# Kernel tuning notes

Measured on AMD Instinct MI355X. Metric: run time of the kernel, lower is better.

The kernel has to match this reference:

```python
import jax, jax.numpy as jnp
import numpy as np

CLAMP = 1e-4


def setup_inputs() -> dict:
    key = jax.random.key(0)
    k1, k2 = jax.random.split(key)
    B, C, H, W = 8, 21, 512, 512
    pred = jax.random.normal(k1, (B, C, H, W), dtype=jnp.float32)
    # valid labels are 1..C-1 (0 = background skipped; class C never appears,
    # matching the original code's loop-with-skip behavior)
    label = jax.random.randint(k2, (B, H, W), 1, C, dtype=jnp.int32)
    return {"pred": pred, "label": label}


def _lovasz(pred, label):
    num_classes = pred.shape[1]
    # [B,C,H,W] -> [N, C], sigmoid + clamp
    p = jnp.transpose(pred, (0, 2, 3, 1)).reshape(-1, num_classes)
    p = jnp.clip(jax.nn.sigmoid(p.astype(jnp.float32)), CLAMP, 1.0 - CLAMP)
    lab = label.reshape(-1)

    # classes 1..num_classes-1 (class num_classes is never present in labels,
    # so its iteration in the original loop always hits `continue`)
    classes = jnp.arange(1, num_classes)
    masks = (lab[None, :] == classes[:, None]).astype(jnp.float32)  # [C-1, N]
    preds_c = p[:, 1:num_classes].T                                  # [C-1, N]

    errors = jnp.abs(masks - preds_c)                                # [C-1, N]
    order = jnp.argsort(-errors, axis=1)                             # descending
    errors_sorted = jnp.take_along_axis(errors, order, axis=1)
    masks_sorted = jnp.take_along_axis(masks, order, axis=1)

    # lovasz_grad, vectorized over classes
    gts = jnp.sum(masks_sorted, axis=1, keepdims=True)               # [C-1, 1]
    intersection = gts - jnp.cumsum(masks_sorted, axis=1)
    union = gts + jnp.cumsum(1.0 - masks_sorted, axis=1)
    jac = 1.0 - intersection / union
    jac = jnp.concatenate([jac[:, :1], jac[:, 1:] - jac[:, :-1]], axis=1)

    per_class = jnp.sum(errors_sorted * jac, axis=1)                 # [C-1]
    present = gts[:, 0] > 0
    count = jnp.sum(present.astype(jnp.float32))
    return jnp.sum(jnp.where(present, per_class, 0.0)) / count


def reference(pred, label):
    return _lovasz(pred, label)
```

## Files before the change

### kernel.cpp

```cpp
#include <hip/hip_runtime.h>

#define NBINS  128
#define NCLS   20
#define CDIM   21
#define HW     (512 * 512)
#define NPIX   (8 * HW)
#define NCHUNK 512
#define CHUNK  (NPIX / NCHUNK)
#define HSZ    (NCLS * NBINS)
#define XSCALE 10.6666667f
#define XBIAS  64.0f

__device__ __forceinline__ float4 gld_f4(const float* p) {
    float4 r;
    asm volatile("global_load_dwordx4 %0, %1, off" : "=v"(r) : "v"(p));
    return r;
}
__device__ __forceinline__ int4 gld_i4(const int* p) {
    int4 r;
    asm volatile("global_load_dwordx4 %0, %1, off" : "=v"(r) : "v"(p));
    return r;
}

__global__ __launch_bounds__(512, 4) void lovasz_hist(const float* __restrict__ pred,
                                                      const int* __restrict__ label,
                                                      unsigned* __restrict__ g_part) {
    __shared__ unsigned s_hist[HSZ];
    const int tid = threadIdx.x;

    const long base = (long)blockIdx.x * CHUNK;
    const int  b    = (int)(base / HW);
    const long hw0  = base - (long)b * HW;
    const float* pbase = pred + ((long)b * CDIM + 1) * HW + hw0 + tid * 4;
    const int*   q     = label + base + tid * 4;

    int4 l[2];
    l[0] = gld_i4(q);
    l[1] = gld_i4(q + 2048);
    float4 buf[3][5];
#pragma unroll
    for (int gg = 0; gg < 2; ++gg)
#pragma unroll
        for (int k = 0; k < 5; ++k)
            buf[gg][k] = gld_f4(pbase + (long)(gg * 5 + k) * HW);

    for (int i = tid; i < HSZ; i += 512) s_hist[i] = 0u;
    __syncthreads();

    auto compute5 = [&](const float4* x, int cbase, const int4& lab) {
#pragma unroll
        for (int j = 0; j < 4; ++j) {
            const int lv = (j == 0) ? lab.x : (j == 1) ? lab.y : (j == 2) ? lab.z : lab.w;
#pragma unroll
            for (int k = 0; k < 5; ++k) {
                const float xv = (j == 0) ? x[k].x : (j == 1) ? x[k].y
                               : (j == 2) ? x[k].z : x[k].w;
                const bool  pos = (lv == cbase + k + 1);
                const float t   = pos ? -xv : xv;
                const float bf  = fminf(fmaxf(__builtin_fmaf(t, XSCALE, XBIAS), 0.0f), 127.0f);
                const int   bin = (int)bf;
                atomicAdd(&s_hist[(cbase + k) * NBINS + bin], pos ? 0x10001u : 1u);
            }
        }
    };

#pragma unroll
    for (int g = 0; g < 8; ++g) {
        if (g + 2 < 8) {
            const int gg = g + 2;
#pragma unroll
            for (int k = 0; k < 5; ++k)
                buf[gg % 3][k] =
                    gld_f4(pbase + (long)((gg & 3) * 5 + k) * HW + (gg >> 2) * 2048);
        }
        if (g < 6)       asm volatile("s_waitcnt vmcnt(10)" ::: "memory");
        else if (g == 6) asm volatile("s_waitcnt vmcnt(5)" ::: "memory");
        else             asm volatile("s_waitcnt vmcnt(0)" ::: "memory");
        __builtin_amdgcn_sched_barrier(0);
        compute5(buf[g % 3], (g & 3) * 5, l[g >> 2]);
    }

    __syncthreads();

    unsigned* gp = g_part + (size_t)blockIdx.x * HSZ;
    for (int i = tid; i < HSZ; i += 512) gp[i] = s_hist[i];
}

__global__ __launch_bounds__(256) void lovasz_reduce(const unsigned* __restrict__ g_part,
                                                     unsigned long long* __restrict__ H) {
    const int t  = threadIdx.x;
    const int i  = blockIdx.x * 16 + (t & 15);
    const int rc = t >> 4;
    const unsigned* gp = g_part + i;

    unsigned vc = 0, vp = 0;
#pragma unroll
    for (int bt = 0; bt < 4; ++bt) {
        unsigned pk = 0;
#pragma unroll
        for (int k = 0; k < 8; ++k)
            pk += gp[(size_t)(rc * 32 + bt * 8 + k) * HSZ];
        vc += pk & 0xFFFFu;
        vp += pk >> 16;
    }
    __shared__ unsigned s_c[16][16], s_p[16][16];
    s_c[rc][t & 15] = vc;
    s_p[rc][t & 15] = vp;
    __syncthreads();
    if (t < 16) {
        unsigned c = 0, p = 0;
#pragma unroll
        for (int r = 0; r < 16; ++r) { c += s_c[r][t]; p += s_p[r][t]; }
        H[blockIdx.x * 16 + t] = (unsigned long long)c | ((unsigned long long)p << 32);
    }
}

__global__ __launch_bounds__(1024) void lovasz_scan(const unsigned long long* __restrict__ H,
                                                    float* __restrict__ out) {
    __shared__ float cls_sum[NCLS];
    __shared__ float cls_cnt[NCLS];
    const int wid  = threadIdx.x >> 6;
    const int lane = threadIdx.x & 63;

#pragma unroll
    for (int it = 0; it < 2; ++it) {
        const int cls = it * 16 + wid;
        if (cls < NCLS) {
            const int bin_lo = 126 - 2 * lane;
            const ulonglong2 v = *reinterpret_cast<const ulonglong2*>(H + cls * NBINS + bin_lo);
            const int vc1 = (int)(v.x & 0xFFFFFFFFull), vp1 = (int)(v.x >> 32);
            const int vc0 = (int)(v.y & 0xFFFFFFFFull), vp0 = (int)(v.y >> 32);
            const int sc = vc0 + vc1, sp = vp0 + vp1;
            int ic = sc, ip = sp;
#pragma unroll
            for (int d = 1; d < 64; d <<= 1) {
                const int tc = __shfl_up(ic, d, 64);
                const int tp = __shfl_up(ip, d, 64);
                if (lane >= d) { ic += tc; ip += tp; }
            }
            const int G   = __shfl(ip, 63, 64);
            const int ec0 = ic - sc, ep0 = ip - sp;
            float contrib = 0.0f;
            if (G > 0) {
                const float fG = (float)G;
                auto J = [&](int i, int m) {
                    return 1.0f - (fG - (float)m) / (fG + (float)(i - m));
                };
                auto EMID = [&](int bn) {
                    const float xm = ((float)bn + 0.5f) * (12.0f / (float)NBINS) - 6.0f;
                    return 1.0f / (1.0f + __expf(-xm));
                };
                if (vc0) {
                    contrib += EMID(127 - 2 * lane) *
                               (J(ec0 + vc0, ep0 + vp0) - J(ec0, ep0));
                }
                if (vc1) {
                    const int ec = ec0 + vc0, ep = ep0 + vp0;
                    contrib += EMID(126 - 2 * lane) *
                               (J(ec + vc1, ep + vp1) - J(ec, ep));
                }
            }
#pragma unroll
            for (int d = 32; d > 0; d >>= 1) contrib += __shfl_down(contrib, d, 64);
            if (lane == 0) {
                cls_sum[cls] = contrib;
                cls_cnt[cls] = (G > 0) ? 1.0f : 0.0f;
            }
        }
    }
    __syncthreads();
    if (threadIdx.x == 0) {
        float s = 0.0f, n = 0.0f;
        for (int c = 0; c < NCLS; ++c) { s += cls_sum[c]; n += cls_cnt[c]; }
        out[0] = s / n;
    }
}

extern "C" void kernel_launch(void* const* d_in, const int* in_sizes, int n_in,
                              void* d_out, int out_size, void* d_ws, size_t ws_size,
                              hipStream_t stream) {
    const float* pred  = (const float*)d_in[0];
    const int*   label = (const int*)d_in[1];

    unsigned* g_part = (unsigned*)d_ws;
    unsigned long long* H = (unsigned long long*)(g_part + (size_t)NCHUNK * HSZ);
    float* out = (float*)d_out;

    lovasz_hist<<<NCHUNK, 512, 0, stream>>>(pred, label, g_part);
    lovasz_reduce<<<HSZ / 16, 256, 0, stream>>>(g_part, H);
    lovasz_scan<<<1, 1024, 0, stream>>>(H, out);
}
```

Measured before the change: 39.99 us.

## Double chunk count, fuse scan into reduce via last-block ticket

The histogram kernel now uses 1024 chunks of one pixel group each, with a two-buffer prefetch and a higher occupancy hint. The reduce kernel uses 320 blocks of 8 bins each, and the last block to finish, chosen by an atomic ticket counter, runs the per-class scan and final average. This drops one kernel launch. The counter is reset by block 0 of the histogram kernel. Trade-offs are twice as many partial histograms to read and write in the reduce, plus fence and atomic overhead.

After: 82.97 us. +107.5%, slower.

```diff
diff --git a/kernel.cpp b/kernel.cpp
--- a/kernel.cpp
+++ b/kernel.cpp
@@ -5,9 +5,10 @@
 #define CDIM   21
 #define HW     (512 * 512)
 #define NPIX   (8 * HW)
-#define NCHUNK 512
+#define NCHUNK 1024
 #define CHUNK  (NPIX / NCHUNK)
 #define HSZ    (NCLS * NBINS)
+#define NRED   320
 #define XSCALE 10.6666667f
 #define XBIAS  64.0f
 
@@ -22,22 +23,21 @@
     return r;
 }
 
-__global__ __launch_bounds__(512, 4) void lovasz_hist(const float* __restrict__ pred,
+__global__ __launch_bounds__(512, 6) void lovasz_hist(const float* __restrict__ pred,
                                                       const int* __restrict__ label,
-                                                      unsigned* __restrict__ g_part) {
+                                                      unsigned* __restrict__ g_part,
+                                                      unsigned* __restrict__ ctr) {
     __shared__ unsigned s_hist[HSZ];
     const int tid = threadIdx.x;
+    if (blockIdx.x == 0 && tid == 0) ctr[0] = 0u;
 
     const long base = (long)blockIdx.x * CHUNK;
     const int  b    = (int)(base / HW);
     const long hw0  = base - (long)b * HW;
     const float* pbase = pred + ((long)b * CDIM + 1) * HW + hw0 + tid * 4;
-    const int*   q     = label + base + tid * 4;
 
-    int4 l[2];
-    l[0] = gld_i4(q);
-    l[1] = gld_i4(q + 2048);
-    float4 buf[3][5];
+    const int4 l = gld_i4(label + base + tid * 4);
+    float4 buf[2][5];
 #pragma unroll
     for (int gg = 0; gg < 2; ++gg)
 #pragma unroll
@@ -47,10 +47,10 @@
     for (int i = tid; i < HSZ; i += 512) s_hist[i] = 0u;
     __syncthreads();
 
-    auto compute5 = [&](const float4* x, int cbase, const int4& lab) {
+    auto compute5 = [&](const float4* x, int cbase) {
 #pragma unroll
         for (int j = 0; j < 4; ++j) {
-            const int lv = (j == 0) ? lab.x : (j == 1) ? lab.y : (j == 2) ? lab.z : lab.w;
+            const int lv = (j == 0) ? l.x : (j == 1) ? l.y : (j == 2) ? l.z : l.w;
 #pragma unroll
             for (int k = 0; k < 5; ++k) {
                 const float xv = (j == 0) ? x[k].x : (j == 1) ? x[k].y
@@ -65,19 +65,16 @@
     };
 
 #pragma unroll
-    for (int g = 0; g < 8; ++g) {
-        if (g + 2 < 8) {
-            const int gg = g + 2;
+    for (int g = 0; g < 4; ++g) {
+        if (g < 3) asm volatile("s_waitcnt vmcnt(5)" ::: "memory");
+        else       asm volatile("s_waitcnt vmcnt(0)" ::: "memory");
+        __builtin_amdgcn_sched_barrier(0);
+        compute5(buf[g & 1], g * 5);
+        if (g + 2 < 4) {
 #pragma unroll
             for (int k = 0; k < 5; ++k)
-                buf[gg % 3][k] =
-                    gld_f4(pbase + (long)((gg & 3) * 5 + k) * HW + (gg >> 2) * 2048);
+                buf[g & 1][k] = gld_f4(pbase + (long)((g + 2) * 5 + k) * HW);
         }
-        if (g < 6)       asm volatile("s_waitcnt vmcnt(10)" ::: "memory");
-        else if (g == 6) asm volatile("s_waitcnt vmcnt(5)" ::: "memory");
-        else             asm volatile("s_waitcnt vmcnt(0)" ::: "memory");
-        __builtin_amdgcn_sched_barrier(0);
-        compute5(buf[g % 3], (g & 3) * 5, l[g >> 2]);
     }
 
     __syncthreads();
@@ -87,11 +84,13 @@
 }
 
 __global__ __launch_bounds__(256) void lovasz_reduce(const unsigned* __restrict__ g_part,
-                                                     unsigned long long* __restrict__ H) {
-    const int t  = threadIdx.x;
-    const int i  = blockIdx.x * 16 + (t & 15);
-    const int rc = t >> 4;
-    const unsigned* gp = g_part + i;
+                                                     unsigned long long* __restrict__ H,
+                                                     unsigned* __restrict__ ctr,
+                                                     float* __restrict__ out) {
+    const int t   = threadIdx.x;
+    const int bin = blockIdx.x * 8 + (t & 7);
+    const int rc  = t >> 3;
+    const unsigned* gp = g_part + bin;
 
     unsigned vc = 0, vp = 0;
 #pragma unroll
@@ -103,73 +102,72 @@
         vc += pk & 0xFFFFu;
         vp += pk >> 16;
     }
-    __shared__ unsigned s_c[16][16], s_p[16][16];
-    s_c[rc][t & 15] = vc;
-    s_p[rc][t & 15] = vp;
+    __shared__ unsigned s_c[32][8], s_p[32][8];
+    s_c[rc][t & 7] = vc;
+    s_p[rc][t & 7] = vp;
     __syncthreads();
-    if (t < 16) {
+    if (t < 8) {
         unsigned c = 0, p = 0;
 #pragma unroll
-        for (int r = 0; r < 16; ++r) { c += s_c[r][t]; p += s_p[r][t]; }
-        H[blockIdx.x * 16 + t] = (unsigned long long)c | ((unsigned long long)p << 32);
+        for (int r = 0; r < 32; ++r) { c += s_c[r][t]; p += s_p[r][t]; }
+        H[blockIdx.x * 8 + t] = (unsigned long long)c | ((unsigned long long)p << 32);
     }
-}
 
-__global__ __launch_bounds__(1024) void lovasz_scan(const unsigned long long* __restrict__ H,
-                                                    float* __restrict__ out) {
-    __shared__ float cls_sum[NCLS];
-    __shared__ float cls_cnt[NCLS];
-    const int wid  = threadIdx.x >> 6;
-    const int lane = threadIdx.x & 63;
+    __threadfence();
+    __syncthreads();
+    __shared__ unsigned s_ticket;
+    if (t == 0) s_ticket = atomicAdd(ctr, 1u);
+    __syncthreads();
+    if (s_ticket != NRED - 1) return;
+    __threadfence();
 
+    __shared__ float cls_sum[NCLS], cls_cnt[NCLS];
+    const int wid  = t >> 6;
+    const int lane = t & 63;
 #pragma unroll
-    for (int it = 0; it < 2; ++it) {
-        const int cls = it * 16 + wid;
-        if (cls < NCLS) {
-            const int bin_lo = 126 - 2 * lane;
-            const ulonglong2 v = *reinterpret_cast<const ulonglong2*>(H + cls * NBINS + bin_lo);
-            const int vc1 = (int)(v.x & 0xFFFFFFFFull), vp1 = (int)(v.x >> 32);
-            const int vc0 = (int)(v.y & 0xFFFFFFFFull), vp0 = (int)(v.y >> 32);
-            const int sc = vc0 + vc1, sp = vp0 + vp1;
-            int ic = sc, ip = sp;
+    for (int it = 0; it < 5; ++it) {
+        const int cls = it * 4 + wid;
+        const int bin_lo = 126 - 2 * lane;
+        const ulonglong2 v = *reinterpret_cast<const ulonglong2*>(H + cls * NBINS + bin_lo);
+        const int vc1 = (int)(v.x & 0xFFFFFFFFull), vp1 = (int)(v.x >> 32);
+        const int vc0 = (int)(v.y & 0xFFFFFFFFull), vp0 = (int)(v.y >> 32);
+        const int sc = vc0 + vc1, sp = vp0 + vp1;
+        int ic = sc, ip = sp;
 #pragma unroll
-            for (int d = 1; d < 64; d <<= 1) {
-                const int tc = __shfl_up(ic, d, 64);
-                const int tp = __shfl_up(ip, d, 64);
-                if (lane >= d) { ic += tc; ip += tp; }
+        for (int d = 1; d < 64; d <<= 1) {
+            const int tc = __shfl_up(ic, d, 64);
+            const int tp = __shfl_up(ip, d, 64);
+            if (lane >= d) { ic += tc; ip += tp; }
+        }
+        const int G   = __shfl(ip, 63, 64);
+        const int ec0 = ic - sc, ep0 = ip - sp;
+        float contrib = 0.0f;
+        if (G > 0) {
+            const float fG = (float)G;
+            auto J = [&](int i, int m) {
+                return 1.0f - (fG - (float)m) / (fG + (float)(i - m));
+            };
+            auto EMID = [&](int bn) {
+                const float xm = ((float)bn + 0.5f) * (12.0f / (float)NBINS) - 6.0f;
+                return 1.0f / (1.0f + __expf(-xm));
+            };
+            if (vc0) contrib += EMID(127 - 2 * lane) *
+                                (J(ec0 + vc0, ep0 + vp0) - J(ec0, ep0));
+            if (vc1) {
+                const int ec = ec0 + vc0, ep = ep0 + vp0;
+                contrib += EMID(126 - 2 * lane) *
+                           (J(ec + vc1, ep + vp1) - J(ec, ep));
             }
-            const int G   = __shfl(ip, 63, 64);
-            const int ec0 = ic - sc, ep0 = ip - sp;
-            float contrib = 0.0f;
-            if (G > 0) {
-                const float fG = (float)G;
-                auto J = [&](int i, int m) {
-                    return 1.0f - (fG - (float)m) / (fG + (float)(i - m));
-                };
-                auto EMID = [&](int bn) {
-                    const float xm = ((float)bn + 0.5f) * (12.0f / (float)NBINS) - 6.0f;
-                    return 1.0f / (1.0f + __expf(-xm));
-                };
-                if (vc0) {
-                    contrib += EMID(127 - 2 * lane) *
-                               (J(ec0 + vc0, ep0 + vp0) - J(ec0, ep0));
-                }
-                if (vc1) {
-                    const int ec = ec0 + vc0, ep = ep0 + vp0;
-                    contrib += EMID(126 - 2 * lane) *
-                               (J(ec + vc1, ep + vp1) - J(ec, ep));
-                }
-            }
+        }
 #pragma unroll
-            for (int d = 32; d > 0; d >>= 1) contrib += __shfl_down(contrib, d, 64);
-            if (lane == 0) {
-                cls_sum[cls] = contrib;
-                cls_cnt[cls] = (G > 0) ? 1.0f : 0.0f;
-            }
+        for (int d = 32; d > 0; d >>= 1) contrib += __shfl_down(contrib, d, 64);
+        if (lane == 0) {
+            cls_sum[cls] = contrib;
+            cls_cnt[cls] = (G > 0) ? 1.0f : 0.0f;
         }
     }
     __syncthreads();
-    if (threadIdx.x == 0) {
+    if (t == 0) {
         float s = 0.0f, n = 0.0f;
         for (int c = 0; c < NCLS; ++c) { s += cls_sum[c]; n += cls_cnt[c]; }
         out[0] = s / n;
@@ -184,9 +182,9 @@
 
     unsigned* g_part = (unsigned*)d_ws;
     unsigned long long* H = (unsigned long long*)(g_part + (size_t)NCHUNK * HSZ);
+    unsigned* ctr = (unsigned*)(H + HSZ);
     float* out = (float*)d_out;
 
-    lovasz_hist<<<NCHUNK, 512, 0, stream>>>(pred, label, g_part);
-    lovasz_reduce<<<HSZ / 16, 256, 0, stream>>>(g_part, H);
-    lovasz_scan<<<1, 1024, 0, stream>>>(H, out);
+    lovasz_hist<<<NCHUNK, 512, 0, stream>>>(pred, label, g_part, ctr);
+    lovasz_reduce<<<NRED, 256, 0, stream>>>(g_part, H, ctr, out);
 }
```
